# Kernel tuning notes

Measured on AMD Instinct MI355X. Metric: run time of the kernel, lower is better.

## Reference

```python
import jax, jax.numpy as jnp
import numpy as np

N_NODES = 100000
N_EDGES = 3200000
IN_F, HID, OUT_F = 256, 128, 8


def gcn_conv(x, src, dst, W, b, n_nodes):
    # PyG GCNConv: linear transform, add self-loops, symmetric normalization, scatter-add, bias
    x = x @ W  # [N, F_out]
    loop = jnp.arange(n_nodes, dtype=src.dtype)
    src_f = jnp.concatenate([src, loop])
    dst_f = jnp.concatenate([dst, loop])
    ones = jnp.ones(src_f.shape[0], dtype=x.dtype)
    deg = jax.ops.segment_sum(ones, dst_f, num_segments=n_nodes)  # in-degree incl self-loop
    dinv = jax.lax.rsqrt(jnp.maximum(deg, 1e-12))
    norm = dinv[src_f] * dinv[dst_f]  # [E+N]
    msgs = x[src_f] * norm[:, None]
    out = jax.ops.segment_sum(msgs, dst_f, num_segments=n_nodes)
    return out + b


def setup_inputs() -> dict:
    key = jax.random.key(0)
    k1, k2, k3, k4 = jax.random.split(key, 4)
    x = jax.random.normal(k1, (N_NODES, IN_F), dtype=jnp.float32)
    edge_index = jax.random.randint(k2, (2, N_EDGES), 0, N_NODES, dtype=jnp.int64)
    W1 = jax.random.normal(k3, (IN_F, HID), dtype=jnp.float32) * (1.0 / np.sqrt(IN_F))
    b1 = jnp.zeros((HID,), dtype=jnp.float32)
    W2 = jax.random.normal(k4, (HID, OUT_F), dtype=jnp.float32) * (1.0 / np.sqrt(HID))
    b2 = jnp.zeros((OUT_F,), dtype=jnp.float32)
    return {"x": x, "edge_index": edge_index, "W1": W1, "b1": b1, "W2": W2, "b2": b2}


def reference(x, edge_index, W1, b1, W2, b2):
    n_nodes = x.shape[0]
    src, dst = edge_index[0], edge_index[1]
    h = gcn_conv(x, src, dst, W1, b1, n_nodes)
    h = jax.nn.relu(h)
    h = gcn_conv(h, src, dst, W2, b2, n_nodes)
    return jax.nn.log_softmax(h, axis=1)
```

## Files before the change

### kernel.cpp

```cpp
#include <hip/hip_runtime.h>
#include <hip/hip_bf16.h>
#include <stdint.h>

#define N_NODES 100000
#define N_EDGES 3200000
#define IN_F 256
#define HID 128
#define OUT_F 8

#define NB   391
#define PASS 6144
#define CAP  10240

typedef short short8 __attribute__((ext_vector_type(8)));
typedef float f32x4 __attribute__((ext_vector_type(4)));
typedef float f32x2 __attribute__((ext_vector_type(2)));

__device__ __forceinline__ uint32_t pk_bf16(float a, float b) {
    uint32_t ua = __float_as_uint(a);
    uint32_t ub = __float_as_uint(b);
    ua = (ua + 0x7fff + ((ua >> 16) & 1)) >> 16;
    ub = (ub + 0x7fff + ((ub >> 16) & 1)) & 0xffff0000u;
    return ua | ub;
}
__device__ __forceinline__ float bl(uint32_t u) { return __uint_as_float(u << 16); }
__device__ __forceinline__ float bh(uint32_t u) { return __uint_as_float(u & 0xffff0000u); }

__device__ __forceinline__ void dec4(uint32_t u, float& a, float& b, float& c, float& d) {
    f32x2 lo = __builtin_amdgcn_cvt_pk_f32_fp8(u, false);
    f32x2 hi = __builtin_amdgcn_cvt_pk_f32_fp8(u, true);
    a = lo[0]; b = lo[1]; c = hi[0]; d = hi[1];
}

__global__ __launch_bounds__(256) void k_bhist(const int* __restrict__ dst,
                                               int* __restrict__ gcnt, int E) {
    __shared__ int lb[NB];
    for (int i = threadIdx.x; i < NB; i += 256) lb[i] = 0;
    __syncthreads();
    int stride = gridDim.x * 256;
    const int4* d4 = (const int4*)dst;
    for (int e = blockIdx.x * 256 + threadIdx.x; e < E / 4; e += stride) {
        int4 d = d4[e];
        atomicAdd(&lb[d.x >> 8], 1);
        atomicAdd(&lb[d.y >> 8], 1);
        atomicAdd(&lb[d.z >> 8], 1);
        atomicAdd(&lb[d.w >> 8], 1);
    }
    __syncthreads();
    for (int i = threadIdx.x; i < NB; i += 256) {
        int c = lb[i];
        if (c) atomicAdd(&gcnt[i * 64], c);
    }
}

__global__ __launch_bounds__(512) void k_bscan(const int* __restrict__ gcnt,
                                               int* __restrict__ bbase,
                                               int* __restrict__ gcur) {
    __shared__ int sc[512];
    int tid = threadIdx.x;
    int v = (tid < NB) ? gcnt[tid * 64] : 0;
    sc[tid] = v;
    __syncthreads();
    for (int d = 1; d < 512; d <<= 1) {
        int t = (tid >= d) ? sc[tid - d] : 0;
        __syncthreads();
        sc[tid] += t;
        __syncthreads();
    }
    int excl = sc[tid] - v;
    if (tid <= NB) bbase[tid] = excl;
    if (tid < NB) gcur[tid * 64] = excl;
}

__global__ __launch_bounds__(256) void k_part(const int* __restrict__ src,
                                              const int* __restrict__ dst,
                                              int* __restrict__ gcur,
                                              uint32_t* __restrict__ epk, int E) {
    __shared__ int lcnt[NB], loff[NB], ladj[NB], lcur[NB];
    __shared__ int sc[512];
    __shared__ uint32_t stage[PASS];
    int tid = threadIdx.x;
    int e0 = blockIdx.x * PASS;

    for (int i = tid; i < NB; i += 256) { lcnt[i] = 0; lcur[i] = 0; }
    __syncthreads();
    for (int i = tid; i < PASS; i += 256) {
        int e = e0 + i;
        if (e < E) atomicAdd(&lcnt[dst[e] >> 8], 1);
    }
    __syncthreads();
    int v0 = (tid < NB) ? lcnt[tid] : 0;
    int v1 = (256 + tid < NB) ? lcnt[256 + tid] : 0;
    sc[tid] = v0; sc[256 + tid] = v1;
    __syncthreads();
    for (int d = 1; d < 512; d <<= 1) {
        int t0 = (tid >= d) ? sc[tid - d] : 0;
        int t1 = (256 + tid >= d) ? sc[256 + tid - d] : 0;
        __syncthreads();
        sc[tid] += t0; sc[256 + tid] += t1;
        __syncthreads();
    }
    if (tid < NB) loff[tid] = sc[tid] - v0;
    if (256 + tid < NB) loff[256 + tid] = sc[256 + tid] - v1;
    __syncthreads();
    for (int b = tid; b < NB; b += 256) {
        int len = lcnt[b];
        if (len > 0) ladj[b] = atomicAdd(&gcur[b * 64], len);
    }
    __syncthreads();
    for (int i = tid; i < PASS; i += 256) {
        int e = e0 + i;
        if (e < E) {
            int d = dst[e];
            int b = d >> 8;
            int r = atomicAdd(&lcur[b], 1);
            stage[loff[b] + r] = (uint32_t)src[e] | ((uint32_t)(d & 255) << 17);
        }
    }
    __syncthreads();
    int wv = tid >> 6, ln = tid & 63;
    for (int b = wv; b < NB; b += 4) {
        int len = lcnt[b], lo = loff[b], gb = ladj[b];
        for (int j = ln; j < len; j += 64) epk[gb + j] = stage[lo + j];
    }
}

__global__ __launch_bounds__(512) void k_csr(const uint32_t* __restrict__ epk,
                                             const int* __restrict__ bbase,
                                             int* __restrict__ offs,
                                             int* __restrict__ cnt,
                                             float* __restrict__ dinv,
                                             int* __restrict__ ssrc, int N) {
    __shared__ int lcnt[256], lcur[256], loff[256];
    __shared__ uint32_t stage[CAP];
    int tid = threadIdx.x, b = blockIdx.x;
    int base = bbase[b], m = bbase[b + 1] - base;

    if (tid < 256) lcnt[tid] = 0;
    __syncthreads();
    for (int i = tid; i < m; i += 512)
        atomicAdd(&lcnt[(epk[base + i] >> 17) & 255], 1);
    __syncthreads();
    int v = (tid < 256) ? lcnt[tid] : 0;
    if (tid < 256) loff[tid] = v;
    __syncthreads();
    for (int d = 1; d < 256; d <<= 1) {
        int t = (tid >= d && tid < 256) ? loff[tid - d] : 0;
        __syncthreads();
        if (tid < 256) loff[tid] += t;
        __syncthreads();
    }
    int excl = (tid < 256) ? (loff[tid] - v) : 0;
    __syncthreads();
    if (tid < 256) {
        loff[tid] = excl;
        lcur[tid] = 0;
        int node = b * 256 + tid;
        if (node < N) {
            offs[node] = base + excl;
            cnt[node] = v;
            dinv[node] = rsqrtf((float)(v + 1));
        }
    }
    __syncthreads();
    if (m <= CAP) {
        for (int i = tid; i < m; i += 512) {
            uint32_t u = epk[base + i];
            int ld = (u >> 17) & 255;
            int r = atomicAdd(&lcur[ld], 1);
            stage[loff[ld] + r] = u & 0x1FFFF;
        }
        __syncthreads();
        for (int i = tid; i < m; i += 512) ssrc[base + i] = (int)stage[i];
    } else {
        for (int i = tid; i < m; i += 512) {
            uint32_t u = epk[base + i];
            int ld = (u >> 17) & 255;
            int r = atomicAdd(&lcur[ld], 1);
            ssrc[base + loff[ld] + r] = (int)(u & 0x1FFFF);
        }
    }
}

__global__ __launch_bounds__(256) void k_wcast(const float* __restrict__ W1,
                                               ushort* __restrict__ Wbf) {
    __shared__ ushort T[128][33];
    int t = threadIdx.x;
    int k0 = blockIdx.x * 32;
    for (int idx = t; idx < 32 * 128; idx += 256) {
        int k = idx >> 7, n = idx & 127;
        uint32_t uv = __float_as_uint(W1[(size_t)(k0 + k) * HID + n]);
        uv = (uv + 0x7fff + ((uv >> 16) & 1)) >> 16;
        T[n][k] = (ushort)uv;
    }
    __syncthreads();
    for (int idx = t; idx < 32 * 128; idx += 256) {
        int n = idx >> 5, k = idx & 31;
        Wbf[(size_t)n * IN_F + k0 + k] = T[n][k];
    }
}

__global__ __launch_bounds__(256) void k_gemm1(const float* __restrict__ X,
                                               const ushort* __restrict__ Wbf,
                                               const float* __restrict__ dinv,
                                               uint32_t* __restrict__ Hs8, int M) {
    __shared__ uint32_t As[64 * 20];
    __shared__ uint32_t Bs[128 * 20];
    __shared__ float st[4][16 * 132];
    int t = threadIdx.x;
    int lane = t & 63, w = t >> 6;
    int q = lane >> 4, c16 = lane & 15;
    int row0 = blockIdx.x * 64;

    int ar = t >> 2, a4 = (t & 3);
    int grow = row0 + ar; if (grow >= M) grow = M - 1;
    const float* xrow = X + (size_t)grow * IN_F;
    int bn = t >> 1, b1h = (t & 1);
    const ushort* wrow = Wbf + (size_t)bn * IN_F;

    f32x4 acc[8];
    #pragma unroll
    for (int j = 0; j < 8; j++) acc[j] = (f32x4){0.f, 0.f, 0.f, 0.f};

    for (int kc = 0; kc < IN_F; kc += 32) {
        float4 x0 = *(const float4*)(xrow + kc + a4 * 8);
        float4 x1 = *(const float4*)(xrow + kc + a4 * 8 + 4);
        uint4 wv0 = *(const uint4*)(wrow + kc + b1h * 16);
        uint4 wv1 = *(const uint4*)(wrow + kc + b1h * 16 + 8);
        __syncthreads();
        *(uint2*)&As[ar * 20 + a4 * 4]     = make_uint2(pk_bf16(x0.x, x0.y), pk_bf16(x0.z, x0.w));
        *(uint2*)&As[ar * 20 + a4 * 4 + 2] = make_uint2(pk_bf16(x1.x, x1.y), pk_bf16(x1.z, x1.w));
        *(uint4*)&Bs[bn * 20 + b1h * 8]     = wv0;
        *(uint4*)&Bs[bn * 20 + b1h * 8 + 4] = wv1;
        __syncthreads();
        short8 af = *(const short8*)&As[(w * 16 + c16) * 20 + q * 4];
        #pragma unroll
        for (int j = 0; j < 8; j++) {
            short8 bf = *(const short8*)&Bs[(j * 16 + c16) * 20 + q * 4];
            acc[j] = __builtin_amdgcn_mfma_f32_16x16x32_bf16(af, bf, acc[j], 0, 0, 0);
        }
    }
    float dv[4];
    #pragma unroll
    for (int r = 0; r < 4; r++) {
        int gr = row0 + w * 16 + q * 4 + r;
        dv[r] = (gr < M) ? dinv[gr] : 0.f;
    }
    #pragma unroll
    for (int j = 0; j < 8; j++)
        #pragma unroll
        for (int r = 0; r < 4; r++)
            st[w][(q * 4 + r) * 132 + j * 16 + c16] = acc[j][r] * dv[r];
    __syncthreads();
    #pragma unroll
    for (int p = 0; p < 4; p++) {
        int rr = p * 4 + q;
        int gr = row0 + w * 16 + rr;
        float4 v0 = *(const float4*)&st[w][rr * 132 + c16 * 8];
        float4 v1 = *(const float4*)&st[w][rr * 132 + c16 * 8 + 4];
        uint32_t lo = 0, hi = 0;
        lo = __builtin_amdgcn_cvt_pk_fp8_f32(v0.x, v0.y, lo, false);
        lo = __builtin_amdgcn_cvt_pk_fp8_f32(v0.z, v0.w, lo, true);
        hi = __builtin_amdgcn_cvt_pk_fp8_f32(v1.x, v1.y, hi, false);
        hi = __builtin_amdgcn_cvt_pk_fp8_f32(v1.z, v1.w, hi, true);
        if (gr < M) *(uint2*)&Hs8[(size_t)gr * 32 + c16 * 2] = make_uint2(lo, hi);
    }
}

__global__ __launch_bounds__(256) void k_agg1(const uint32_t* __restrict__ hs,
                                              const int* __restrict__ offs,
                                              const int* __restrict__ cnt,
                                              const float* __restrict__ dinv,
                                              const int* __restrict__ ssrc,
                                              const float* __restrict__ b1,
                                              uint32_t* __restrict__ a1, int N) {
    int wid = (blockIdx.x * 256 + threadIdx.x) >> 6;
    int lane = threadIdx.x & 63;
    if (wid >= N) return;
    int h = lane >> 5, c = lane & 31;
    float dv = dinv[wid];
    float s0f = 0.f, s1f = 0.f, s2f = 0.f, s3f = 0.f;
    if (h == 0) {
        dec4(hs[(size_t)wid * 32 + c], s0f, s1f, s2f, s3f);
    }
    int beg = offs[wid], n = cnt[wid];
    const int* sp = ssrc + beg;
    int j = h;
    float x0, x1, x2, x3;
    for (; j + 14 < n; j += 16) {
        int e0 = sp[j],      e1 = sp[j + 2],  e2 = sp[j + 4],  e3 = sp[j + 6];
        int e4 = sp[j + 8],  e5 = sp[j + 10], e6 = sp[j + 12], e7 = sp[j + 14];
        uint32_t u0 = hs[(size_t)e0 * 32 + c];
        uint32_t u1 = hs[(size_t)e1 * 32 + c];
        uint32_t u2 = hs[(size_t)e2 * 32 + c];
        uint32_t u3 = hs[(size_t)e3 * 32 + c];
        uint32_t u4 = hs[(size_t)e4 * 32 + c];
        uint32_t u5 = hs[(size_t)e5 * 32 + c];
        uint32_t u6 = hs[(size_t)e6 * 32 + c];
        uint32_t u7 = hs[(size_t)e7 * 32 + c];
        dec4(u0, x0, x1, x2, x3); s0f += x0; s1f += x1; s2f += x2; s3f += x3;
        dec4(u1, x0, x1, x2, x3); s0f += x0; s1f += x1; s2f += x2; s3f += x3;
        dec4(u2, x0, x1, x2, x3); s0f += x0; s1f += x1; s2f += x2; s3f += x3;
        dec4(u3, x0, x1, x2, x3); s0f += x0; s1f += x1; s2f += x2; s3f += x3;
        dec4(u4, x0, x1, x2, x3); s0f += x0; s1f += x1; s2f += x2; s3f += x3;
        dec4(u5, x0, x1, x2, x3); s0f += x0; s1f += x1; s2f += x2; s3f += x3;
        dec4(u6, x0, x1, x2, x3); s0f += x0; s1f += x1; s2f += x2; s3f += x3;
        dec4(u7, x0, x1, x2, x3); s0f += x0; s1f += x1; s2f += x2; s3f += x3;
    }
    for (; j + 6 < n; j += 8) {
        int e0 = sp[j], e1 = sp[j + 2], e2 = sp[j + 4], e3 = sp[j + 6];
        uint32_t u0 = hs[(size_t)e0 * 32 + c];
        uint32_t u1 = hs[(size_t)e1 * 32 + c];
        uint32_t u2 = hs[(size_t)e2 * 32 + c];
        uint32_t u3 = hs[(size_t)e3 * 32 + c];
        dec4(u0, x0, x1, x2, x3); s0f += x0; s1f += x1; s2f += x2; s3f += x3;
        dec4(u1, x0, x1, x2, x3); s0f += x0; s1f += x1; s2f += x2; s3f += x3;
        dec4(u2, x0, x1, x2, x3); s0f += x0; s1f += x1; s2f += x2; s3f += x3;
        dec4(u3, x0, x1, x2, x3); s0f += x0; s1f += x1; s2f += x2; s3f += x3;
    }
    for (; j < n; j += 2) {
        uint32_t u = hs[(size_t)sp[j] * 32 + c];
        dec4(u, x0, x1, x2, x3); s0f += x0; s1f += x1; s2f += x2; s3f += x3;
    }
    s0f += __shfl_xor(s0f, 32);
    s1f += __shfl_xor(s1f, 32);
    s2f += __shfl_xor(s2f, 32);
    s3f += __shfl_xor(s3f, 32);
    if (h == 0) {
        float4 bb = *(const float4*)(b1 + c * 4);
        float o0 = fmaxf(fmaf(s0f, dv, bb.x), 0.f);
        float o1 = fmaxf(fmaf(s1f, dv, bb.y), 0.f);
        float o2 = fmaxf(fmaf(s2f, dv, bb.z), 0.f);
        float o3 = fmaxf(fmaf(s3f, dv, bb.w), 0.f);
        *(uint2*)&a1[(size_t)wid * 64 + c * 2] = make_uint2(pk_bf16(o0, o1), pk_bf16(o2, o3));
    }
}

__global__ __launch_bounds__(256) void k_gemm2(const uint32_t* __restrict__ a1,
                                               const float* __restrict__ W2,
                                               const float* __restrict__ dinv,
                                               float* __restrict__ h2s, int N) {
    __shared__ float w[HID * OUT_F];
    int t = threadIdx.x;
    for (int i = t; i < HID * OUT_F; i += 256) w[i] = W2[i];
    __syncthreads();
    int node = blockIdx.x * 32 + (t >> 3);
    int f = t & 7;
    if (node >= N) return;
    const uint32_t* ar = a1 + (size_t)node * 64;
    float acc = 0.f;
    #pragma unroll 8
    for (int k = 0; k < 64; k++) {
        uint32_t u = ar[k];
        acc = fmaf(bl(u), w[(2 * k) * OUT_F + f], acc);
        acc = fmaf(bh(u), w[(2 * k + 1) * OUT_F + f], acc);
    }
    h2s[(size_t)node * OUT_F + f] = acc * dinv[node];
}

__global__ __launch_bounds__(256) void k_agg2(const float* __restrict__ h2s,
                                              const int* __restrict__ offs,
                                              const int* __restrict__ cnt,
                                              const float* __restrict__ dinv,
                                              const int* __restrict__ ssrc,
                                              const float* __restrict__ b2,
                                              float* __restrict__ out, int N) {
    int wid = (blockIdx.x * 256 + threadIdx.x) >> 6;
    int lane = threadIdx.x & 63;
    if (wid >= N) return;
    int f = lane & 7, g = lane >> 3;
    float dv = dinv[wid];
    int beg = offs[wid], n = cnt[wid];
    float acc = 0.f;
    for (int j = g; j < n; j += 8) {
        int s = ssrc[beg + j];
        acc += h2s[(size_t)s * OUT_F + f];
    }
    acc += __shfl_xor(acc, 8);
    acc += __shfl_xor(acc, 16);
    acc += __shfl_xor(acc, 32);
    acc += h2s[(size_t)wid * OUT_F + f];
    acc = fmaf(acc, dv, b2[f]);
    float m = acc;
    m = fmaxf(m, __shfl_xor(m, 1));
    m = fmaxf(m, __shfl_xor(m, 2));
    m = fmaxf(m, __shfl_xor(m, 4));
    float e = expf(acc - m);
    float ssum = e;
    ssum += __shfl_xor(ssum, 1);
    ssum += __shfl_xor(ssum, 2);
    ssum += __shfl_xor(ssum, 4);
    float res = acc - m - logf(ssum);
    if (lane < 8) out[(size_t)wid * OUT_F + lane] = res;
}

extern "C" void kernel_launch(void* const* d_in, const int* in_sizes, int n_in,
                              void* d_out, int out_size, void* d_ws, size_t ws_size,
                              hipStream_t stream) {
    const float* x   = (const float*)d_in[0];
    const int*   ei  = (const int*)d_in[1];
    const float* W1  = (const float*)d_in[2];
    const float* b1  = (const float*)d_in[3];
    const float* W2  = (const float*)d_in[4];
    const float* b2  = (const float*)d_in[5];
    float* out = (float*)d_out;

    const int N = N_NODES, E = N_EDGES;
    const int* src = ei;
    const int* dst = ei + E;

    char* p = (char*)d_ws;
    auto carve = [&](size_t bytes) -> void* {
        void* r = (void*)p;
        p += (bytes + 511) & ~(size_t)511;
        return r;
    };
    int*      gcnt  = (int*)carve((size_t)NB * 64 * 4);
    int*      gcur  = (int*)carve((size_t)NB * 64 * 4);
    int*      bbase = (int*)carve((size_t)(NB + 1) * 4);
    uint32_t* epk   = (uint32_t*)carve((size_t)E * 4);
    int*      offs  = (int*)carve((size_t)N * 4);
    int*      cnt   = (int*)carve((size_t)N * 4);
    float*    dinv  = (float*)carve((size_t)N * 4);
    int*      ssrc  = (int*)carve((size_t)E * 4);
    ushort*   wbf   = (ushort*)carve((size_t)HID * IN_F * 2);
    uint32_t* hs8   = (uint32_t*)carve((size_t)N * 32 * 4);
    uint32_t* a1    = (uint32_t*)carve((size_t)N * 64 * 4);
    float*    h2s   = (float*)carve((size_t)N * OUT_F * 4);

    hipMemsetAsync(gcnt, 0, (size_t)NB * 64 * 4, stream);

    k_wcast<<<8, 256, 0, stream>>>(W1, wbf);
    k_bhist<<<512, 256, 0, stream>>>(dst, gcnt, E);
    k_bscan<<<1, 512, 0, stream>>>(gcnt, bbase, gcur);
    k_part<<<(E + PASS - 1) / PASS, 256, 0, stream>>>(src, dst, gcur, epk, E);
    k_csr<<<NB, 512, 0, stream>>>(epk, bbase, offs, cnt, dinv, ssrc, N);

    k_gemm1<<<(N + 63) / 64, 256, 0, stream>>>(x, wbf, dinv, hs8, N);
    k_agg1<<<(N * 64 + 255) / 256, 256, 0, stream>>>(hs8, offs, cnt, dinv, ssrc, b1, a1, N);
    k_gemm2<<<(N + 31) / 32, 256, 0, stream>>>(a1, W2, dinv, h2s, N);
    k_agg2<<<(N * 64 + 255) / 256, 256, 0, stream>>>(h2s, offs, cnt, dinv, ssrc, b2, out, N);
}
```

Baseline: 406.3 us.

## Fuse layer-2 GEMM into first aggregation and widen partition/CSR blocks

The second linear transform (128->8) now happens inside the first aggregation kernel through a lane-parallel dot product and shuffle reduction. This removes the bf16 a1 intermediate and the separate k_gemm2 launch. The partition and CSR-build kernels run with twice as many threads per block, and the layer-2 aggregation loop is unrolled four-way to keep more gathers in flight. The fused kernel adds shared-memory W2 staging and a longer shuffle reduction per node, and drops the bf16 rounding of the hidden activations.

```diff
diff --git a/kernel.cpp b/kernel.cpp
--- a/kernel.cpp
+++ b/kernel.cpp
@@ -22,14 +22,6 @@
     ua = (ua + 0x7fff + ((ua >> 16) & 1)) >> 16;
     ub = (ub + 0x7fff + ((ub >> 16) & 1)) & 0xffff0000u;
     return ua | ub;
-}
-__device__ __forceinline__ float bl(uint32_t u) { return __uint_as_float(u << 16); }
-__device__ __forceinline__ float bh(uint32_t u) { return __uint_as_float(u & 0xffff0000u); }
-
-__device__ __forceinline__ void dec4(uint32_t u, float& a, float& b, float& c, float& d) {
-    f32x2 lo = __builtin_amdgcn_cvt_pk_f32_fp8(u, false);
-    f32x2 hi = __builtin_amdgcn_cvt_pk_f32_fp8(u, true);
-    a = lo[0]; b = lo[1]; c = hi[0]; d = hi[1];
 }
 
 __global__ __launch_bounds__(256) void k_bhist(const int* __restrict__ dst,
@@ -72,7 +64,7 @@
     if (tid < NB) gcur[tid * 64] = excl;
 }
 
-__global__ __launch_bounds__(256) void k_part(const int* __restrict__ src,
+__global__ __launch_bounds__(512) void k_part(const int* __restrict__ src,
                                               const int* __restrict__ dst,
                                               int* __restrict__ gcur,
                                               uint32_t* __restrict__ epk, int E) {
@@ -82,33 +74,30 @@
     int tid = threadIdx.x;
     int e0 = blockIdx.x * PASS;
 
-    for (int i = tid; i < NB; i += 256) { lcnt[i] = 0; lcur[i] = 0; }
-    __syncthreads();
-    for (int i = tid; i < PASS; i += 256) {
+    for (int i = tid; i < NB; i += 512) { lcnt[i] = 0; lcur[i] = 0; }
+    __syncthreads();
+    for (int i = tid; i < PASS; i += 512) {
         int e = e0 + i;
         if (e < E) atomicAdd(&lcnt[dst[e] >> 8], 1);
     }
     __syncthreads();
-    int v0 = (tid < NB) ? lcnt[tid] : 0;
-    int v1 = (256 + tid < NB) ? lcnt[256 + tid] : 0;
-    sc[tid] = v0; sc[256 + tid] = v1;
+    int v = (tid < NB) ? lcnt[tid] : 0;
+    sc[tid] = v;
     __syncthreads();
     for (int d = 1; d < 512; d <<= 1) {
-        int t0 = (tid >= d) ? sc[tid - d] : 0;
-        int t1 = (256 + tid >= d) ? sc[256 + tid - d] : 0;
-        __syncthreads();
-        sc[tid] += t0; sc[256 + tid] += t1;
-        __syncthreads();
-    }
-    if (tid < NB) loff[tid] = sc[tid] - v0;
-    if (256 + tid < NB) loff[256 + tid] = sc[256 + tid] - v1;
-    __syncthreads();
-    for (int b = tid; b < NB; b += 256) {
-        int len = lcnt[b];
-        if (len > 0) ladj[b] = atomicAdd(&gcur[b * 64], len);
-    }
-    __syncthreads();
-    for (int i = tid; i < PASS; i += 256) {
+        int t = (tid >= d) ? sc[tid - d] : 0;
+        __syncthreads();
+        sc[tid] += t;
+        __syncthreads();
+    }
+    if (tid < NB) loff[tid] = sc[tid] - v;
+    __syncthreads();
+    if (tid < NB) {
+        int len = lcnt[tid];
+        if (len > 0) ladj[tid] = atomicAdd(&gcur[tid * 64], len);
+    }
+    __syncthreads();
+    for (int i = tid; i < PASS; i += 512) {
         int e = e0 + i;
         if (e < E) {
             int d = dst[e];
@@ -119,18 +108,18 @@
     }
     __syncthreads();
     int wv = tid >> 6, ln = tid & 63;
-    for (int b = wv; b < NB; b += 4) {
+    for (int b = wv; b < NB; b += 8) {
         int len = lcnt[b], lo = loff[b], gb = ladj[b];
         for (int j = ln; j < len; j += 64) epk[gb + j] = stage[lo + j];
     }
 }
 
-__global__ __launch_bounds__(512) void k_csr(const uint32_t* __restrict__ epk,
-                                             const int* __restrict__ bbase,
-                                             int* __restrict__ offs,
-                                             int* __restrict__ cnt,
-                                             float* __restrict__ dinv,
-                                             int* __restrict__ ssrc, int N) {
+__global__ __launch_bounds__(1024) void k_csr(const uint32_t* __restrict__ epk,
+                                              const int* __restrict__ bbase,
+                                              int* __restrict__ offs,
+                                              int* __restrict__ cnt,
+                                              float* __restrict__ dinv,
+                                              int* __restrict__ ssrc, int N) {
     __shared__ int lcnt[256], lcur[256], loff[256];
     __shared__ uint32_t stage[CAP];
     int tid = threadIdx.x, b = blockIdx.x;
@@ -138,7 +127,7 @@
 
     if (tid < 256) lcnt[tid] = 0;
     __syncthreads();
-    for (int i = tid; i < m; i += 512)
+    for (int i = tid; i < m; i += 1024)
         atomicAdd(&lcnt[(epk[base + i] >> 17) & 255], 1);
     __syncthreads();
     int v = (tid < 256) ? lcnt[tid] : 0;
@@ -164,16 +153,16 @@
     }
     __syncthreads();
     if (m <= CAP) {
-        for (int i = tid; i < m; i += 512) {
+        for (int i = tid; i < m; i += 1024) {
             uint32_t u = epk[base + i];
             int ld = (u >> 17) & 255;
             int r = atomicAdd(&lcur[ld], 1);
             stage[loff[ld] + r] = u & 0x1FFFF;
         }
         __syncthreads();
-        for (int i = tid; i < m; i += 512) ssrc[base + i] = (int)stage[i];
+        for (int i = tid; i < m; i += 1024) ssrc[base + i] = (int)stage[i];
     } else {
-        for (int i = tid; i < m; i += 512) {
+        for (int i = tid; i < m; i += 1024) {
             uint32_t u = epk[base + i];
             int ld = (u >> 17) & 255;
             int r = atomicAdd(&lcur[ld], 1);
@@ -273,20 +262,29 @@
                                               const float* __restrict__ dinv,
                                               const int* __restrict__ ssrc,
                                               const float* __restrict__ b1,
-                                              uint32_t* __restrict__ a1, int N) {
-    int wid = (blockIdx.x * 256 + threadIdx.x) >> 6;
-    int lane = threadIdx.x & 63;
+                                              const float* __restrict__ W2,
+                                              float* __restrict__ h2s, int N) {
+    __shared__ float w2t[OUT_F * HID];
+    int t = threadIdx.x;
+    for (int i = t; i < OUT_F * HID; i += 256) {
+        int f = i & 7, k = i >> 3;
+        w2t[f * HID + k] = W2[k * OUT_F + f];
+    }
+    __syncthreads();
+    int wid = (blockIdx.x * 256 + t) >> 6;
+    int lane = t & 63;
     if (wid >= N) return;
     int h = lane >> 5, c = lane & 31;
     float dv = dinv[wid];
-    float s0f = 0.f, s1f = 0.f, s2f = 0.f, s3f = 0.f;
+    f32x2 s01 = {0.f, 0.f}, s23 = {0.f, 0.f};
     if (h == 0) {
-        dec4(hs[(size_t)wid * 32 + c], s0f, s1f, s2f, s3f);
+        uint32_t u = hs[(size_t)wid * 32 + c];
+        s01 = __builtin_amdgcn_cvt_pk_f32_fp8(u, false);
+        s23 = __builtin_amdgcn_cvt_pk_f32_fp8(u, true);
     }
     int beg = offs[wid], n = cnt[wid];
     const int* sp = ssrc + beg;
     int j = h;
-    float x0, x1, x2, x3;
     for (; j + 14 < n; j += 16) {
         int e0 = sp[j],      e1 = sp[j + 2],  e2 = sp[j + 4],  e3 = sp[j + 6];
         int e4 = sp[j + 8],  e5 = sp[j + 10], e6 = sp[j + 12], e7 = sp[j + 14];
@@ -298,14 +296,14 @@
         uint32_t u5 = hs[(size_t)e5 * 32 + c];
         uint32_t u6 = hs[(size_t)e6 * 32 + c];
         uint32_t u7 = hs[(size_t)e7 * 32 + c];
-        dec4(u0, x0, x1, x2, x3); s0f += x0; s1f += x1; s2f += x2; s3f += x3;
-        dec4(u1, x0, x1, x2, x3); s0f += x0; s1f += x1; s2f += x2; s3f += x3;
-        dec4(u2, x0, x1, x2, x3); s0f += x0; s1f += x1; s2f += x2; s3f += x3;
-        dec4(u3, x0, x1, x2, x3); s0f += x0; s1f += x1; s2f += x2; s3f += x3;
-        dec4(u4, x0, x1, x2, x3); s0f += x0; s1f += x1; s2f += x2; s3f += x3;
-        dec4(u5, x0, x1, x2, x3); s0f += x0; s1f += x1; s2f += x2; s3f += x3;
-        dec4(u6, x0, x1, x2, x3); s0f += x0; s1f += x1; s2f += x2; s3f += x3;
-        dec4(u7, x0, x1, x2, x3); s0f += x0; s1f += x1; s2f += x2; s3f += x3;
+        s01 += __builtin_amdgcn_cvt_pk_f32_fp8(u0, false); s23 += __builtin_amdgcn_cvt_pk_f32_fp8(u0, true);
+        s01 += __builtin_amdgcn_cvt_pk_f32_fp8(u1, false); s23 += __builtin_amdgcn_cvt_pk_f32_fp8(u1, true);
+        s01 += __builtin_amdgcn_cvt_pk_f32_fp8(u2, false); s23 += __builtin_amdgcn_cvt_pk_f32_fp8(u2, true);
+        s01 += __builtin_amdgcn_cvt_pk_f32_fp8(u3, false); s23 += __builtin_amdgcn_cvt_pk_f32_fp8(u3, true);
+        s01 += __builtin_amdgcn_cvt_pk_f32_fp8(u4, false); s23 += __builtin_amdgcn_cvt_pk_f32_fp8(u4, true);
+        s01 += __builtin_amdgcn_cvt_pk_f32_fp8(u5, false); s23 += __builtin_amdgcn_cvt_pk_f32_fp8(u5, true);
+        s01 += __builtin_amdgcn_cvt_pk_f32_fp8(u6, false); s23 += __builtin_amdgcn_cvt_pk_f32_fp8(u6, true);
+        s01 += __builtin_amdgcn_cvt_pk_f32_fp8(u7, false); s23 += __builtin_amdgcn_cvt_pk_f32_fp8(u7, true);
     }
     for (; j + 6 < n; j += 8) {
         int e0 = sp[j], e1 = sp[j + 2], e2 = sp[j + 4], e3 = sp[j + 6];
@@ -313,49 +311,41 @@
         uint32_t u1 = hs[(size_t)e1 * 32 + c];
         uint32_t u2 = hs[(size_t)e2 * 32 + c];
         uint32_t u3 = hs[(size_t)e3 * 32 + c];
-        dec4(u0, x0, x1, x2, x3); s0f += x0; s1f += x1; s2f += x2; s3f += x3;
-        dec4(u1, x0, x1, x2, x3); s0f += x0; s1f += x1; s2f += x2; s3f += x3;
-        dec4(u2, x0, x1, x2, x3); s0f += x0; s1f += x1; s2f += x2; s3f += x3;
-        dec4(u3, x0, x1, x2, x3); s0f += x0; s1f += x1; s2f += x2; s3f += x3;
+        s01 += __builtin_amdgcn_cvt_pk_f32_fp8(u0, false); s23 += __builtin_amdgcn_cvt_pk_f32_fp8(u0, true);
+        s01 += __builtin_amdgcn_cvt_pk_f32_fp8(u1, false); s23 += __builtin_amdgcn_cvt_pk_f32_fp8(u1, true);
+        s01 += __builtin_amdgcn_cvt_pk_f32_fp8(u2, false); s23 += __builtin_amdgcn_cvt_pk_f32_fp8(u2, true);
+        s01 += __builtin_amdgcn_cvt_pk_f32_fp8(u3, false); s23 += __builtin_amdgcn_cvt_pk_f32_fp8(u3, true);
     }
     for (; j < n; j += 2) {
         uint32_t u = hs[(size_t)sp[j] * 32 + c];
-        dec4(u, x0, x1, x2, x3); s0f += x0; s1f += x1; s2f += x2; s3f += x3;
-    }
-    s0f += __shfl_xor(s0f, 32);
-    s1f += __shfl_xor(s1f, 32);
-    s2f += __shfl_xor(s2f, 32);
-    s3f += __shfl_xor(s3f, 32);
-    if (h == 0) {
-        float4 bb = *(const float4*)(b1 + c * 4);
-        float o0 = fmaxf(fmaf(s0f, dv, bb.x), 0.f);
-        float o1 = fmaxf(fmaf(s1f, dv, bb.y), 0.f);
-        float o2 = fmaxf(fmaf(s2f, dv, bb.z), 0.f);
-        float o3 = fmaxf(fmaf(s3f, dv, bb.w), 0.f);
-        *(uint2*)&a1[(size_t)wid * 64 + c * 2] = make_uint2(pk_bf16(o0, o1), pk_bf16(o2, o3));
-    }
-}
-
-__global__ __launch_bounds__(256) void k_gemm2(const uint32_t* __restrict__ a1,
-                                               const float* __restrict__ W2,
-                                               const float* __restrict__ dinv,
-                                               float* __restrict__ h2s, int N) {
-    __shared__ float w[HID * OUT_F];
-    int t = threadIdx.x;
-    for (int i = t; i < HID * OUT_F; i += 256) w[i] = W2[i];
-    __syncthreads();
-    int node = blockIdx.x * 32 + (t >> 3);
-    int f = t & 7;
-    if (node >= N) return;
-    const uint32_t* ar = a1 + (size_t)node * 64;
-    float acc = 0.f;
-    #pragma unroll 8
-    for (int k = 0; k < 64; k++) {
-        uint32_t u = ar[k];
-        acc = fmaf(bl(u), w[(2 * k) * OUT_F + f], acc);
-        acc = fmaf(bh(u), w[(2 * k + 1) * OUT_F + f], acc);
-    }
-    h2s[(size_t)node * OUT_F + f] = acc * dinv[node];
+        s01 += __builtin_amdgcn_cvt_pk_f32_fp8(u, false);
+        s23 += __builtin_amdgcn_cvt_pk_f32_fp8(u, true);
+    }
+    s01[0] += __shfl_xor(s01[0], 32);
+    s01[1] += __shfl_xor(s01[1], 32);
+    s23[0] += __shfl_xor(s23[0], 32);
+    s23[1] += __shfl_xor(s23[1], 32);
+    float4 bb = *(const float4*)(b1 + c * 4);
+    float o0 = fmaxf(fmaf(s01[0], dv, bb.x), 0.f);
+    float o1 = fmaxf(fmaf(s01[1], dv, bb.y), 0.f);
+    float o2 = fmaxf(fmaf(s23[0], dv, bb.z), 0.f);
+    float o3 = fmaxf(fmaf(s23[1], dv, bb.w), 0.f);
+    int f0 = h * 4;
+    float p[4];
+    #pragma unroll
+    for (int f = 0; f < 4; f++) {
+        float4 wv = *(const float4*)&w2t[(f0 + f) * HID + c * 4];
+        p[f] = o0 * wv.x + o1 * wv.y + o2 * wv.z + o3 * wv.w;
+    }
+    #pragma unroll
+    for (int d = 1; d < 32; d <<= 1) {
+        #pragma unroll
+        for (int f = 0; f < 4; f++) p[f] += __shfl_xor(p[f], d);
+    }
+    if (c == 0) {
+        float4 ov = make_float4(p[0] * dv, p[1] * dv, p[2] * dv, p[3] * dv);
+        *(float4*)&h2s[(size_t)wid * OUT_F + f0] = ov;
+    }
 }
 
 __global__ __launch_bounds__(256) void k_agg2(const float* __restrict__ h2s,
@@ -371,11 +361,18 @@
     int f = lane & 7, g = lane >> 3;
     float dv = dinv[wid];
     int beg = offs[wid], n = cnt[wid];
+    const int* sp = ssrc + beg;
     float acc = 0.f;
-    for (int j = g; j < n; j += 8) {
-        int s = ssrc[beg + j];
-        acc += h2s[(size_t)s * OUT_F + f];
-    }
+    int j = g;
+    for (; j + 24 < n; j += 32) {
+        int s0 = sp[j], s1 = sp[j + 8], s2 = sp[j + 16], s3 = sp[j + 24];
+        float v0 = h2s[(size_t)s0 * OUT_F + f];
+        float v1 = h2s[(size_t)s1 * OUT_F + f];
+        float v2 = h2s[(size_t)s2 * OUT_F + f];
+        float v3 = h2s[(size_t)s3 * OUT_F + f];
+        acc += v0 + v1 + v2 + v3;
+    }
+    for (; j < n; j += 8) acc += h2s[(size_t)sp[j] * OUT_F + f];
     acc += __shfl_xor(acc, 8);
     acc += __shfl_xor(acc, 16);
     acc += __shfl_xor(acc, 32);
@@ -425,7 +422,6 @@
     int*      ssrc  = (int*)carve((size_t)E * 4);
     ushort*   wbf   = (ushort*)carve((size_t)HID * IN_F * 2);
     uint32_t* hs8   = (uint32_t*)carve((size_t)N * 32 * 4);
-    uint32_t* a1    = (uint32_t*)carve((size_t)N * 64 * 4);
     float*    h2s   = (float*)carve((size_t)N * OUT_F * 4);
 
     hipMemsetAsync(gcnt, 0, (size_t)NB * 64 * 4, stream);
@@ -433,11 +429,10 @@
     k_wcast<<<8, 256, 0, stream>>>(W1, wbf);
     k_bhist<<<512, 256, 0, stream>>>(dst, gcnt, E);
     k_bscan<<<1, 512, 0, stream>>>(gcnt, bbase, gcur);
-    k_part<<<(E + PASS - 1) / PASS, 256, 0, stream>>>(src, dst, gcur, epk, E);
-    k_csr<<<NB, 512, 0, stream>>>(epk, bbase, offs, cnt, dinv, ssrc, N);
+    k_part<<<(E + PASS - 1) / PASS, 512, 0, stream>>>(src, dst, gcur, epk, E);
+    k_csr<<<NB, 1024, 0, stream>>>(epk, bbase, offs, cnt, dinv, ssrc, N);
 
     k_gemm1<<<(N + 63) / 64, 256, 0, stream>>>(x, wbf, dinv, hs8, N);
-    k_agg1<<<(N * 64 + 255) / 256, 256, 0, stream>>>(hs8, offs, cnt, dinv, ssrc, b1, a1, N);
-    k_gemm2<<<(N + 31) / 32, 256, 0, stream>>>(a1, W2, dinv, h2s, N);
+    k_agg1<<<(N * 64 + 255) / 256, 256, 0, stream>>>(hs8, offs, cnt, dinv, ssrc, b1, W2, h2s, N);
     k_agg2<<<(N * 64 + 255) / 256, 256, 0, stream>>>(h2s, offs, cnt, dinv, ssrc, b2, out, N);
 }
```

Measured after the change: 379.2 us. -6.7%, faster.
